# Kernel optimization log

Measured on AMD Instinct MI355X. Metric: run time of the kernel, lower is better.

Reference implementation:

```python
import jax, jax.numpy as jnp
import numpy as np

N_Q = 8
N_LAYERS = 3
SCALE = np.pi / 2


def _apply_1q(state, gate, q):
    # state: (B, 2,...,2) [N_Q qubit axes]; gate: (2,2) shared or (B,2,2) batched
    B = state.shape[0]
    s = jnp.moveaxis(state, 1 + q, 1).reshape(B, 2, -1)
    if gate.ndim == 2:
        s = jnp.einsum('ij,bjk->bik', gate, s)
    else:
        s = jnp.einsum('bij,bjk->bik', gate, s)
    s = s.reshape((B,) + (2,) * N_Q)
    return jnp.moveaxis(s, 1, 1 + q)


def _apply_cnot(state, c, t):
    # flip target axis within the control=1 slice
    s = jnp.moveaxis(state, (1 + c, 1 + t), (1, 2))
    s = jnp.concatenate([s[:, :1], jnp.flip(s[:, 1:], axis=2)], axis=1)
    return jnp.moveaxis(s, (1, 2), (1 + c, 1 + t))


def _ry(theta):
    # RY(t) = [[cos(t/2), -sin(t/2)], [sin(t/2), cos(t/2)]]; theta: (...,)
    c = jnp.cos(theta / 2)
    s = jnp.sin(theta / 2)
    m = jnp.stack([jnp.stack([c, -s], -1), jnp.stack([s, c], -1)], -2)
    return m.astype(jnp.complex64)


def _rz(phi):
    # RZ(p) = diag(exp(-ip/2), exp(ip/2))
    e = jnp.exp(-0.5j * phi.astype(jnp.complex64))
    z = jnp.zeros_like(e)
    return jnp.stack([jnp.stack([e, z], -1), jnp.stack([z, jnp.conj(e)], -1)], -2)


def _circuit(angles, theta, phi):
    # angles: (B, N_Q); theta, phi: (N_LAYERS, N_Q) -> Z expectations (B, N_Q)
    B = angles.shape[0]
    state = jnp.zeros((B, 2 ** N_Q), jnp.complex64).at[:, 0].set(1.0)
    state = state.reshape((B,) + (2,) * N_Q)
    enc = _ry(angles)  # (B, N_Q, 2, 2), batch-dependent encoding gates
    for q in range(N_Q):
        state = _apply_1q(state, enc[:, q], q)
    ryg = _ry(theta)  # (L, N_Q, 2, 2)
    rzg = _rz(phi)
    for l in range(N_LAYERS):
        for q in range(N_Q):
            state = _apply_1q(state, ryg[l, q], q)
        for q in range(N_Q):
            state = _apply_cnot(state, q, (q + 1) % N_Q)
        for q in range(N_Q):
            state = _apply_1q(state, rzg[l, q], q)
    probs = state.real ** 2 + state.imag ** 2  # (B, 2,...,2)
    z = []
    for q in range(N_Q):
        p = jnp.moveaxis(probs, 1 + q, 1).reshape(B, 2, -1).sum(-1)
        z.append(p[:, 0] - p[:, 1])
    return jnp.stack(z, axis=1)  # (B, N_Q)


def setup_inputs() -> dict:
    key = jax.random.key(0)
    ks = jax.random.split(key, 5)
    B, D, H = 16384, 256, 128
    x = jax.random.normal(ks[0], (B, D), dtype=jnp.float32)
    theta = jax.random.normal(ks[1], (N_LAYERS, N_Q), dtype=jnp.float32) * 0.1
    phi = jax.random.normal(ks[2], (N_LAYERS, N_Q), dtype=jnp.float32) * 0.1
    W1 = jax.random.normal(ks[3], (N_Q, H), dtype=jnp.float32) * (1.0 / np.sqrt(N_Q))
    b1 = jnp.zeros((H,), jnp.float32)
    W2 = jax.random.normal(ks[4], (H, D), dtype=jnp.float32) * (1.0 / np.sqrt(H))
    b2 = jnp.zeros((D,), jnp.float32)
    return {"x": x, "theta": theta, "phi": phi, "W1": W1, "b1": b1, "W2": W2, "b2": b2}


def reference(x, theta, phi, W1, b1, W2, b2):
    # per-sample min-max normalization (original calls _amplitude_encode on x[i:i+1])
    fmin = x.min(axis=1, keepdims=True)
    fmax = x.max(axis=1, keepdims=True)
    angles = (x[:, :N_Q] - fmin) / (fmax - fmin + 1e-8) * SCALE
    q = _circuit(angles, theta, phi)  # (B, 8) Pauli-Z expectations
    h = jax.nn.relu(q @ W1 + b1)
    transformed = h @ W2 + b2
    return x + transformed
```

## Files before the change

### kernel.cpp

```cpp
#include <hip/hip_runtime.h>
#include <hip/hip_bf16.h>

typedef __attribute__((ext_vector_type(8))) short short8;
typedef __attribute__((ext_vector_type(4))) float float4v;

#define PSTRIDE   260
#define PSISTRIDE 264
#define HSTRIDE   136

__device__ __forceinline__ float shflx(float v, int m) {
    return __shfl_xor(v, m, 64);
}

__device__ __forceinline__ unsigned short f2bf(float f) {
    union { __hip_bfloat16 h; unsigned short u; } cv;
    cv.h = __float2bfloat16(f);
    return cv.u;
}

__global__ __launch_bounds__(256) void vqc_build_u_kernel(
    const float* __restrict__ theta,
    const float* __restrict__ phi,
    const float* __restrict__ W2,
    unsigned short* __restrict__ Bmat,
    unsigned short* __restrict__ W2T)
{
    const int b = blockIdx.x;
    if (b >= 64) {
        const int k0 = (b - 64) * 4;
        const int n = threadIdx.x;
        ushort4 pk;
        pk.x = f2bf(W2[(k0 + 0) * 256 + n]);
        pk.y = f2bf(W2[(k0 + 1) * 256 + n]);
        pk.z = f2bf(W2[(k0 + 2) * 256 + n]);
        pk.w = f2bf(W2[(k0 + 3) * 256 + n]);
        *reinterpret_cast<ushort4*>(W2T + n * 128 + k0) = pk;
        return;
    }
    const int lane = threadIdx.x & 63;
    const int j = (b << 2) + (threadIdx.x >> 6);

    float re[4], im[4];
    #pragma unroll
    for (int jj = 0; jj < 4; ++jj) {
        re[jj] = (lane * 4 + jj == j) ? 1.f : 0.f;
        im[jj] = 0.f;
    }

    for (int l = 0; l < 3; ++l) {
        #pragma unroll
        for (int q = 0; q < 6; ++q) {
            float th = 0.5f * theta[l * 8 + q];
            float ct = __cosf(th), st = __sinf(th);
            float sg = ((lane >> (5 - q)) & 1) ? st : -st;
            const int m = 1 << (5 - q);
            #pragma unroll
            for (int jj = 0; jj < 4; ++jj) {
                float orr = shflx(re[jj], m), oi = shflx(im[jj], m);
                re[jj] = fmaf(ct, re[jj], sg * orr);
                im[jj] = fmaf(ct, im[jj], sg * oi);
            }
        }
        {
            float th = 0.5f * theta[l * 8 + 6];
            float ct = __cosf(th), st = __sinf(th);
            #pragma unroll
            for (int jj = 0; jj < 2; ++jj) {
                float r0 = re[jj], i0 = im[jj], r1 = re[jj + 2], i1 = im[jj + 2];
                re[jj]     = fmaf(ct, r0, -st * r1);
                im[jj]     = fmaf(ct, i0, -st * i1);
                re[jj + 2] = fmaf(ct, r1,  st * r0);
                im[jj + 2] = fmaf(ct, i1,  st * i0);
            }
        }
        {
            float th = 0.5f * theta[l * 8 + 7];
            float ct = __cosf(th), st = __sinf(th);
            #pragma unroll
            for (int jj = 0; jj < 4; jj += 2) {
                float r0 = re[jj], i0 = im[jj], r1 = re[jj + 1], i1 = im[jj + 1];
                re[jj]     = fmaf(ct, r0, -st * r1);
                im[jj]     = fmaf(ct, i0, -st * i1);
                re[jj + 1] = fmaf(ct, r1,  st * r0);
                im[jj + 1] = fmaf(ct, i1,  st * i0);
            }
        }
        #pragma unroll
        for (int q = 0; q < 5; ++q) {
            const int tm = 1 << (4 - q);
            const bool cb = (lane >> (5 - q)) & 1;
            #pragma unroll
            for (int jj = 0; jj < 4; ++jj) {
                float orr = shflx(re[jj], tm), oi = shflx(im[jj], tm);
                re[jj] = cb ? orr : re[jj];
                im[jj] = cb ? oi  : im[jj];
            }
        }
        {   const bool cb = lane & 1;
            float t;
            t = re[0]; re[0] = cb ? re[2] : re[0]; re[2] = cb ? t : re[2];
            t = im[0]; im[0] = cb ? im[2] : im[0]; im[2] = cb ? t : im[2];
            t = re[1]; re[1] = cb ? re[3] : re[1]; re[3] = cb ? t : re[3];
            t = im[1]; im[1] = cb ? im[3] : im[1]; im[3] = cb ? t : im[3];
        }
        {   float t;
            t = re[2]; re[2] = re[3]; re[3] = t;
            t = im[2]; im[2] = im[3]; im[3] = t;
        }
        {
            re[1] = shflx(re[1], 32); im[1] = shflx(im[1], 32);
            re[3] = shflx(re[3], 32); im[3] = shflx(im[3], 32);
        }
        float al = 0.f;
        #pragma unroll
        for (int q = 0; q < 6; ++q) {
            float h = 0.5f * phi[l * 8 + q];
            al += ((lane >> (5 - q)) & 1) ? h : -h;
        }
        float h6 = 0.5f * phi[l * 8 + 6], h7 = 0.5f * phi[l * 8 + 7];
        float ajs[4] = { al - h6 - h7, al - h6 + h7, al + h6 - h7, al + h6 + h7 };
        #pragma unroll
        for (int jj = 0; jj < 4; ++jj) {
            float cc = __cosf(ajs[jj]), sn = __sinf(ajs[jj]);
            float r = re[jj], i = im[jj];
            re[jj] = r * cc - i * sn;
            im[jj] = fmaf(r, sn, i * cc);
        }
    }

    #pragma unroll
    for (int jj = 0; jj < 4; ++jj) {
        int kp = lane * 4 + jj;
        Bmat[(size_t)kp * 256 + j]         = f2bf(re[jj]);
        Bmat[(size_t)(kp + 256) * 256 + j] = f2bf(im[jj]);
    }
}

__global__ __launch_bounds__(256) void vqc_mega_kernel(
    const float* __restrict__ x,
    const unsigned short* __restrict__ Bmat,
    const unsigned short* __restrict__ W2T,
    const float* __restrict__ W1,
    const float* __restrict__ b1,
    const float* __restrict__ b2,
    float* __restrict__ out,
    int B)
{
    __shared__ __align__(16) char smem[32 * PSTRIDE * 4];
    __shared__ float z_lds[32][8];
    float (*p_lds)[PSTRIDE] = (float(*)[PSTRIDE])smem;
    unsigned short (*psi_lds)[PSISTRIDE] = (unsigned short(*)[PSISTRIDE])smem;
    unsigned short (*h_lds)[HSTRIDE] = (unsigned short(*)[HSTRIDE])smem;

    const int t = threadIdx.x;
    const int lane = t & 63;
    const int w = t >> 6;
    const int c = lane & 15;
    const int quad = lane >> 4;
    const int s0 = blockIdx.x * 32;

    {
        const int g = t >> 3;
        const int sub = t & 7;
        const float4* xr = reinterpret_cast<const float4*>(x + (size_t)(s0 + g) * 256) + sub * 8;
        float4 v0 = xr[0], v1 = xr[1], v2 = xr[2], v3 = xr[3];
        float4 v4 = xr[4], v5 = xr[5], v6 = xr[6], v7 = xr[7];
        float mn = fminf(fminf(fminf(v0.x, v0.y), fminf(v0.z, v0.w)),
                         fminf(fminf(v1.x, v1.y), fminf(v1.z, v1.w)));
        mn = fminf(mn, fminf(fminf(fminf(v2.x, v2.y), fminf(v2.z, v2.w)),
                             fminf(fminf(v3.x, v3.y), fminf(v3.z, v3.w))));
        mn = fminf(mn, fminf(fminf(fminf(v4.x, v4.y), fminf(v4.z, v4.w)),
                             fminf(fminf(v5.x, v5.y), fminf(v5.z, v5.w))));
        mn = fminf(mn, fminf(fminf(fminf(v6.x, v6.y), fminf(v6.z, v6.w)),
                             fminf(fminf(v7.x, v7.y), fminf(v7.z, v7.w))));
        float mx = fmaxf(fmaxf(fmaxf(v0.x, v0.y), fmaxf(v0.z, v0.w)),
                         fmaxf(fmaxf(v1.x, v1.y), fmaxf(v1.z, v1.w)));
        mx = fmaxf(mx, fmaxf(fmaxf(fmaxf(v2.x, v2.y), fmaxf(v2.z, v2.w)),
                             fmaxf(fmaxf(v3.x, v3.y), fmaxf(v3.z, v3.w))));
        mx = fmaxf(mx, fmaxf(fmaxf(fmaxf(v4.x, v4.y), fmaxf(v4.z, v4.w)),
                             fmaxf(fmaxf(v5.x, v5.y), fmaxf(v5.z, v5.w))));
        mx = fmaxf(mx, fmaxf(fmaxf(fmaxf(v6.x, v6.y), fmaxf(v6.z, v6.w)),
                             fmaxf(fmaxf(v7.x, v7.y), fmaxf(v7.z, v7.w))));
        #pragma unroll
        for (int m = 1; m < 8; m <<= 1) {
            mn = fminf(mn, shflx(mn, m));
            mx = fmaxf(mx, shflx(mx, m));
        }
        const float scale = 0.78539816339744831f / (mx - mn + 1e-8f);

        const int base = lane & 56;
        float xq[8];
        xq[0] = __shfl(v0.x, base); xq[1] = __shfl(v0.y, base);
        xq[2] = __shfl(v0.z, base); xq[3] = __shfl(v0.w, base);
        xq[4] = __shfl(v1.x, base); xq[5] = __shfl(v1.y, base);
        xq[6] = __shfl(v1.z, base); xq[7] = __shfl(v1.w, base);

        float cq[8], sq[8];
        #pragma unroll
        for (int q = 0; q < 8; ++q) {
            float a = (xq[q] - mn) * scale;
            cq[q] = __cosf(a);
            sq[q] = __sinf(a);
        }
        float pref = ((sub >> 2) & 1 ? sq[0] : cq[0]) *
                     ((sub >> 1) & 1 ? sq[1] : cq[1]) *
                     ((sub >> 0) & 1 ? sq[2] : cq[2]);
        float p1[2], p2[4], p3[8], p4[16];
        p1[0] = pref * cq[3]; p1[1] = pref * sq[3];
        #pragma unroll
        for (int i = 0; i < 2; ++i) { p2[2*i] = p1[i] * cq[4]; p2[2*i+1] = p1[i] * sq[4]; }
        #pragma unroll
        for (int i = 0; i < 4; ++i) { p3[2*i] = p2[i] * cq[5]; p3[2*i+1] = p2[i] * sq[5]; }
        #pragma unroll
        for (int i = 0; i < 8; ++i) { p4[2*i] = p3[i] * cq[6]; p4[2*i+1] = p3[i] * sq[6]; }
        ushort2* dst = reinterpret_cast<ushort2*>(&psi_lds[g][sub * 32]);
        #pragma unroll
        for (int i = 0; i < 16; ++i) {
            ushort2 pk;
            pk.x = f2bf(p4[i] * cq[7]);
            pk.y = f2bf(p4[i] * sq[7]);
            dst[i] = pk;
        }
    }
    __syncthreads();

    float4v acc[2][8];
    #pragma unroll
    for (int h = 0; h < 2; ++h)
        #pragma unroll
        for (int tt = 0; tt < 8; ++tt)
            acc[h][tt] = (float4v){0.f, 0.f, 0.f, 0.f};

    #pragma unroll
    for (int kk = 0; kk < 8; ++kk) {
        const int ko = kk * 32 + quad * 8;
        short8 a0 = *(const short8*)(&psi_lds[c][ko]);
        short8 a1 = *(const short8*)(&psi_lds[16 + c][ko]);
        #pragma unroll
        for (int tt = 0; tt < 4; ++tt) {
            const int nr = (w * 4 + tt) * 16 + c;
            short8 bre = *(const short8*)(Bmat + (size_t)nr * 256 + ko);
            short8 bim = *(const short8*)(Bmat + (size_t)(nr + 256) * 256 + ko);
            acc[0][tt]     = __builtin_amdgcn_mfma_f32_16x16x32_bf16(a0, bre, acc[0][tt], 0, 0, 0);
            acc[1][tt]     = __builtin_amdgcn_mfma_f32_16x16x32_bf16(a1, bre, acc[1][tt], 0, 0, 0);
            acc[0][tt + 4] = __builtin_amdgcn_mfma_f32_16x16x32_bf16(a0, bim, acc[0][tt + 4], 0, 0, 0);
            acc[1][tt + 4] = __builtin_amdgcn_mfma_f32_16x16x32_bf16(a1, bim, acc[1][tt + 4], 0, 0, 0);
        }
    }
    __syncthreads();

    #pragma unroll
    for (int h = 0; h < 2; ++h)
        #pragma unroll
        for (int tt = 0; tt < 4; ++tt) {
            const int n = (w * 4 + tt) * 16 + c;
            #pragma unroll
            for (int r = 0; r < 4; ++r) {
                const int m = h * 16 + quad * 4 + r;
                const float pr = acc[h][tt][r], pi = acc[h][tt + 4][r];
                p_lds[m][n] = pr * pr + pi * pi;
            }
        }
    __syncthreads();

    {
        const int m = t >> 3, q = t & 7, sh = 7 - q;
        const float4* prow = (const float4*)&p_lds[m][0];
        float zv = 0.f;
        #pragma unroll 8
        for (int n4 = 0; n4 < 64; ++n4) {
            float4 pv = prow[n4];
            const int n = n4 * 4;
            zv += (((n + 0) >> sh) & 1) ? -pv.x : pv.x;
            zv += (((n + 1) >> sh) & 1) ? -pv.y : pv.y;
            zv += (((n + 2) >> sh) & 1) ? -pv.z : pv.z;
            zv += (((n + 3) >> sh) & 1) ? -pv.w : pv.w;
        }
        z_lds[m][q] = zv;
    }
    __syncthreads();

    {
        const int j = t & 127, ig = t >> 7;
        float w1v[8];
        #pragma unroll
        for (int q = 0; q < 8; ++q) w1v[q] = W1[q * 128 + j];
        const float b1v = b1[j];
        #pragma unroll
        for (int ii = 0; ii < 16; ++ii) {
            const int i = ig * 16 + ii;
            float a = b1v;
            #pragma unroll
            for (int q = 0; q < 8; ++q) a = fmaf(z_lds[i][q], w1v[q], a);
            h_lds[i][j] = f2bf(fmaxf(a, 0.f));
        }
    }
    __syncthreads();

    float4v acc2[2][4];
    #pragma unroll
    for (int h = 0; h < 2; ++h)
        #pragma unroll
        for (int tt = 0; tt < 4; ++tt)
            acc2[h][tt] = (float4v){0.f, 0.f, 0.f, 0.f};

    #pragma unroll
    for (int kk = 0; kk < 4; ++kk) {
        const int ko = kk * 32 + quad * 8;
        short8 a0 = *(const short8*)(&h_lds[c][ko]);
        short8 a1 = *(const short8*)(&h_lds[16 + c][ko]);
        #pragma unroll
        for (int tt = 0; tt < 4; ++tt) {
            const int nr = (w * 4 + tt) * 16 + c;
            short8 bw = *(const short8*)(W2T + (size_t)nr * 128 + ko);
            acc2[0][tt] = __builtin_amdgcn_mfma_f32_16x16x32_bf16(a0, bw, acc2[0][tt], 0, 0, 0);
            acc2[1][tt] = __builtin_amdgcn_mfma_f32_16x16x32_bf16(a1, bw, acc2[1][tt], 0, 0, 0);
        }
    }

    #pragma unroll
    for (int h = 0; h < 2; ++h)
        #pragma unroll
        for (int tt = 0; tt < 4; ++tt) {
            const int n = (w * 4 + tt) * 16 + c;
            const float b2v = b2[n];
            #pragma unroll
            for (int r = 0; r < 4; ++r) {
                const int m = h * 16 + quad * 4 + r;
                const size_t idx = (size_t)(s0 + m) * 256 + n;
                out[idx] = x[idx] + b2v + acc2[h][tt][r];
            }
        }
}

extern "C" void kernel_launch(void* const* d_in, const int* in_sizes, int n_in,
                              void* d_out, int out_size, void* d_ws, size_t ws_size,
                              hipStream_t stream) {
    const float* x     = (const float*)d_in[0];
    const float* theta = (const float*)d_in[1];
    const float* phi   = (const float*)d_in[2];
    const float* W1    = (const float*)d_in[3];
    const float* b1    = (const float*)d_in[4];
    const float* W2    = (const float*)d_in[5];
    const float* b2    = (const float*)d_in[6];
    float* out = (float*)d_out;
    const int B = in_sizes[0] / 256;

    unsigned short* Bmat = (unsigned short*)d_ws;
    unsigned short* W2T  = Bmat + 512 * 256;

    vqc_build_u_kernel<<<dim3(96), dim3(256), 0, stream>>>(theta, phi, W2, Bmat, W2T);
    vqc_mega_kernel<<<dim3(B / 32), dim3(256), 0, stream>>>(
        x, Bmat, W2T, W1, b1, b2, out, B);
}
```

Before: 108.2 us.

## Process 64 samples per 1024-thread block and restructure Z reduction

```diff
diff --git a/kernel.cpp b/kernel.cpp
--- a/kernel.cpp
+++ b/kernel.cpp
@@ -4,9 +4,10 @@
 typedef __attribute__((ext_vector_type(8))) short short8;
 typedef __attribute__((ext_vector_type(4))) float float4v;
 
-#define PSTRIDE   260
-#define PSISTRIDE 264
-#define HSTRIDE   136
+#define NS    64
+#define PSTR  264
+#define HSTR  136
+#define ZPSTR 68
 
 __device__ __forceinline__ float shflx(float v, int m) {
     return __shfl_xor(v, m, 64);
@@ -16,6 +17,12 @@
     union { __hip_bfloat16 h; unsigned short u; } cv;
     cv.h = __float2bfloat16(f);
     return cv.u;
+}
+
+__device__ __forceinline__ float bfbits(unsigned int u) {
+    union { unsigned int u; float f; } cv;
+    cv.u = u;
+    return cv.f;
 }
 
 __global__ __launch_bounds__(256) void vqc_build_u_kernel(
@@ -61,8 +68,7 @@
                 im[jj] = fmaf(ct, im[jj], sg * oi);
             }
         }
-        {
-            float th = 0.5f * theta[l * 8 + 6];
+        {   float th = 0.5f * theta[l * 8 + 6];
             float ct = __cosf(th), st = __sinf(th);
             #pragma unroll
             for (int jj = 0; jj < 2; ++jj) {
@@ -73,8 +79,7 @@
                 im[jj + 2] = fmaf(ct, i1,  st * i0);
             }
         }
-        {
-            float th = 0.5f * theta[l * 8 + 7];
+        {   float th = 0.5f * theta[l * 8 + 7];
             float ct = __cosf(th), st = __sinf(th);
             #pragma unroll
             for (int jj = 0; jj < 4; jj += 2) {
@@ -107,8 +112,7 @@
             t = re[2]; re[2] = re[3]; re[3] = t;
             t = im[2]; im[2] = im[3]; im[3] = t;
         }
-        {
-            re[1] = shflx(re[1], 32); im[1] = shflx(im[1], 32);
+        {   re[1] = shflx(re[1], 32); im[1] = shflx(im[1], 32);
             re[3] = shflx(re[3], 32); im[3] = shflx(im[3], 32);
         }
         float al = 0.f;
@@ -136,59 +140,50 @@
     }
 }
 
-__global__ __launch_bounds__(256) void vqc_mega_kernel(
+__global__ __launch_bounds__(1024) void vqc_mega_kernel(
     const float* __restrict__ x,
     const unsigned short* __restrict__ Bmat,
     const unsigned short* __restrict__ W2T,
     const float* __restrict__ W1,
     const float* __restrict__ b1,
     const float* __restrict__ b2,
-    float* __restrict__ out,
-    int B)
+    float* __restrict__ out)
 {
-    __shared__ __align__(16) char smem[32 * PSTRIDE * 4];
-    __shared__ float z_lds[32][8];
-    float (*p_lds)[PSTRIDE] = (float(*)[PSTRIDE])smem;
-    unsigned short (*psi_lds)[PSISTRIDE] = (unsigned short(*)[PSISTRIDE])smem;
-    unsigned short (*h_lds)[HSTRIDE] = (unsigned short(*)[HSTRIDE])smem;
+    __shared__ __align__(16) unsigned short region[NS * PSTR];
+    __shared__ __align__(16) float zp_lds[NS * ZPSTR];
+    __shared__ float z_lds[NS][8];
+
+    unsigned short (*psi)[PSTR]  = (unsigned short(*)[PSTR])region;
+    unsigned short (*hmat)[HSTR] = (unsigned short(*)[HSTR])region;
 
     const int t = threadIdx.x;
     const int lane = t & 63;
     const int w = t >> 6;
     const int c = lane & 15;
     const int quad = lane >> 4;
-    const int s0 = blockIdx.x * 32;
+    const int s0 = blockIdx.x * NS;
 
     {
-        const int g = t >> 3;
-        const int sub = t & 7;
-        const float4* xr = reinterpret_cast<const float4*>(x + (size_t)(s0 + g) * 256) + sub * 8;
+        const int g = t >> 4;
+        const int sub = t & 15;
+        const float4* xr = reinterpret_cast<const float4*>(x + (size_t)(s0 + g) * 256) + sub * 4;
         float4 v0 = xr[0], v1 = xr[1], v2 = xr[2], v3 = xr[3];
-        float4 v4 = xr[4], v5 = xr[5], v6 = xr[6], v7 = xr[7];
         float mn = fminf(fminf(fminf(v0.x, v0.y), fminf(v0.z, v0.w)),
                          fminf(fminf(v1.x, v1.y), fminf(v1.z, v1.w)));
         mn = fminf(mn, fminf(fminf(fminf(v2.x, v2.y), fminf(v2.z, v2.w)),
                              fminf(fminf(v3.x, v3.y), fminf(v3.z, v3.w))));
-        mn = fminf(mn, fminf(fminf(fminf(v4.x, v4.y), fminf(v4.z, v4.w)),
-                             fminf(fminf(v5.x, v5.y), fminf(v5.z, v5.w))));
-        mn = fminf(mn, fminf(fminf(fminf(v6.x, v6.y), fminf(v6.z, v6.w)),
-                             fminf(fminf(v7.x, v7.y), fminf(v7.z, v7.w))));
         float mx = fmaxf(fmaxf(fmaxf(v0.x, v0.y), fmaxf(v0.z, v0.w)),
                          fmaxf(fmaxf(v1.x, v1.y), fmaxf(v1.z, v1.w)));
         mx = fmaxf(mx, fmaxf(fmaxf(fmaxf(v2.x, v2.y), fmaxf(v2.z, v2.w)),
                              fmaxf(fmaxf(v3.x, v3.y), fmaxf(v3.z, v3.w))));
-        mx = fmaxf(mx, fmaxf(fmaxf(fmaxf(v4.x, v4.y), fmaxf(v4.z, v4.w)),
-                             fmaxf(fmaxf(v5.x, v5.y), fmaxf(v5.z, v5.w))));
-        mx = fmaxf(mx, fmaxf(fmaxf(fmaxf(v6.x, v6.y), fmaxf(v6.z, v6.w)),
-                             fmaxf(fmaxf(v7.x, v7.y), fmaxf(v7.z, v7.w))));
-        #pragma unroll
-        for (int m = 1; m < 8; m <<= 1) {
+        #pragma unroll
+        for (int m = 1; m < 16; m <<= 1) {
             mn = fminf(mn, shflx(mn, m));
             mx = fmaxf(mx, shflx(mx, m));
         }
         const float scale = 0.78539816339744831f / (mx - mn + 1e-8f);
 
-        const int base = lane & 56;
+        const int base = lane & 48;
         float xq[8];
         xq[0] = __shfl(v0.x, base); xq[1] = __shfl(v0.y, base);
         xq[2] = __shfl(v0.z, base); xq[3] = __shfl(v0.w, base);
@@ -202,80 +197,105 @@
             cq[q] = __cosf(a);
             sq[q] = __sinf(a);
         }
-        float pref = ((sub >> 2) & 1 ? sq[0] : cq[0]) *
-                     ((sub >> 1) & 1 ? sq[1] : cq[1]) *
-                     ((sub >> 0) & 1 ? sq[2] : cq[2]);
-        float p1[2], p2[4], p3[8], p4[16];
-        p1[0] = pref * cq[3]; p1[1] = pref * sq[3];
-        #pragma unroll
-        for (int i = 0; i < 2; ++i) { p2[2*i] = p1[i] * cq[4]; p2[2*i+1] = p1[i] * sq[4]; }
-        #pragma unroll
-        for (int i = 0; i < 4; ++i) { p3[2*i] = p2[i] * cq[5]; p3[2*i+1] = p2[i] * sq[5]; }
-        #pragma unroll
-        for (int i = 0; i < 8; ++i) { p4[2*i] = p3[i] * cq[6]; p4[2*i+1] = p3[i] * sq[6]; }
-        ushort2* dst = reinterpret_cast<ushort2*>(&psi_lds[g][sub * 32]);
-        #pragma unroll
-        for (int i = 0; i < 16; ++i) {
-            ushort2 pk;
-            pk.x = f2bf(p4[i] * cq[7]);
-            pk.y = f2bf(p4[i] * sq[7]);
-            dst[i] = pk;
-        }
-    }
-    __syncthreads();
-
-    float4v acc[2][8];
-    #pragma unroll
-    for (int h = 0; h < 2; ++h)
-        #pragma unroll
-        for (int tt = 0; tt < 8; ++tt)
-            acc[h][tt] = (float4v){0.f, 0.f, 0.f, 0.f};
-
+        float pref = ((sub & 8) ? sq[0] : cq[0]) *
+                     ((sub & 4) ? sq[1] : cq[1]) *
+                     ((sub & 2) ? sq[2] : cq[2]) *
+                     ((sub & 1) ? sq[3] : cq[3]);
+        float p1[2], p2[4], p3[8];
+        p1[0] = pref * cq[4]; p1[1] = pref * sq[4];
+        #pragma unroll
+        for (int i = 0; i < 2; ++i) { p2[2*i] = p1[i] * cq[5]; p2[2*i+1] = p1[i] * sq[5]; }
+        #pragma unroll
+        for (int i = 0; i < 4; ++i) { p3[2*i] = p2[i] * cq[6]; p3[2*i+1] = p2[i] * sq[6]; }
+        #pragma unroll
+        for (int i = 0; i < 4; ++i) {
+            ushort4 pk;
+            pk.x = f2bf(p3[2*i]     * cq[7]);
+            pk.y = f2bf(p3[2*i]     * sq[7]);
+            pk.z = f2bf(p3[2*i + 1] * cq[7]);
+            pk.w = f2bf(p3[2*i + 1] * sq[7]);
+            *reinterpret_cast<ushort4*>(&psi[g][sub * 16 + 4 * i]) = pk;
+        }
+    }
+    __syncthreads();
+
+    float4v accre[4], accim[4];
+    #pragma unroll
+    for (int mt = 0; mt < 4; ++mt) {
+        accre[mt] = (float4v){0.f, 0.f, 0.f, 0.f};
+        accim[mt] = (float4v){0.f, 0.f, 0.f, 0.f};
+    }
     #pragma unroll
     for (int kk = 0; kk < 8; ++kk) {
         const int ko = kk * 32 + quad * 8;
-        short8 a0 = *(const short8*)(&psi_lds[c][ko]);
-        short8 a1 = *(const short8*)(&psi_lds[16 + c][ko]);
-        #pragma unroll
-        for (int tt = 0; tt < 4; ++tt) {
-            const int nr = (w * 4 + tt) * 16 + c;
-            short8 bre = *(const short8*)(Bmat + (size_t)nr * 256 + ko);
-            short8 bim = *(const short8*)(Bmat + (size_t)(nr + 256) * 256 + ko);
-            acc[0][tt]     = __builtin_amdgcn_mfma_f32_16x16x32_bf16(a0, bre, acc[0][tt], 0, 0, 0);
-            acc[1][tt]     = __builtin_amdgcn_mfma_f32_16x16x32_bf16(a1, bre, acc[1][tt], 0, 0, 0);
-            acc[0][tt + 4] = __builtin_amdgcn_mfma_f32_16x16x32_bf16(a0, bim, acc[0][tt + 4], 0, 0, 0);
-            acc[1][tt + 4] = __builtin_amdgcn_mfma_f32_16x16x32_bf16(a1, bim, acc[1][tt + 4], 0, 0, 0);
-        }
-    }
-    __syncthreads();
-
-    #pragma unroll
-    for (int h = 0; h < 2; ++h)
-        #pragma unroll
-        for (int tt = 0; tt < 4; ++tt) {
-            const int n = (w * 4 + tt) * 16 + c;
-            #pragma unroll
-            for (int r = 0; r < 4; ++r) {
-                const int m = h * 16 + quad * 4 + r;
-                const float pr = acc[h][tt][r], pi = acc[h][tt + 4][r];
-                p_lds[m][n] = pr * pr + pi * pi;
-            }
-        }
-    __syncthreads();
-
-    {
-        const int m = t >> 3, q = t & 7, sh = 7 - q;
-        const float4* prow = (const float4*)&p_lds[m][0];
+        short8 a0 = *(const short8*)(&psi[c][ko]);
+        short8 a1 = *(const short8*)(&psi[16 + c][ko]);
+        short8 a2 = *(const short8*)(&psi[32 + c][ko]);
+        short8 a3 = *(const short8*)(&psi[48 + c][ko]);
+        short8 bre = *(const short8*)(Bmat + (size_t)(w * 16 + c) * 256 + ko);
+        short8 bim = *(const short8*)(Bmat + (size_t)(256 + w * 16 + c) * 256 + ko);
+        accre[0] = __builtin_amdgcn_mfma_f32_16x16x32_bf16(a0, bre, accre[0], 0, 0, 0);
+        accre[1] = __builtin_amdgcn_mfma_f32_16x16x32_bf16(a1, bre, accre[1], 0, 0, 0);
+        accre[2] = __builtin_amdgcn_mfma_f32_16x16x32_bf16(a2, bre, accre[2], 0, 0, 0);
+        accre[3] = __builtin_amdgcn_mfma_f32_16x16x32_bf16(a3, bre, accre[3], 0, 0, 0);
+        accim[0] = __builtin_amdgcn_mfma_f32_16x16x32_bf16(a0, bim, accim[0], 0, 0, 0);
+        accim[1] = __builtin_amdgcn_mfma_f32_16x16x32_bf16(a1, bim, accim[1], 0, 0, 0);
+        accim[2] = __builtin_amdgcn_mfma_f32_16x16x32_bf16(a2, bim, accim[2], 0, 0, 0);
+        accim[3] = __builtin_amdgcn_mfma_f32_16x16x32_bf16(a3, bim, accim[3], 0, 0, 0);
+    }
+    __syncthreads();
+
+    #pragma unroll
+    for (int mt = 0; mt < 4; ++mt)
+        #pragma unroll
+        for (int r = 0; r < 4; ++r) {
+            const int m = mt * 16 + quad * 4 + r;
+            const float pr = accre[mt][r], pi = accim[mt][r];
+            psi[m][w * 16 + c] = f2bf(pr * pr + pi * pi);
+        }
+    __syncthreads();
+
+    if (t < 512) {
+        const int m = t >> 3, h = t & 7;
+        const uint4* pu = (const uint4*)(&psi[m][h * 32]);
+        float s[8], d6s = 0.f, d7s = 0.f;
+        #pragma unroll
+        for (int i = 0; i < 4; ++i) {
+            uint4 u = pu[i];
+            {   float e0 = bfbits(u.x << 16), e1 = bfbits(u.x & 0xffff0000u);
+                float e2 = bfbits(u.y << 16), e3 = bfbits(u.y & 0xffff0000u);
+                float a01 = e0 + e1, a23 = e2 + e3;
+                s[2*i] = a01 + a23;
+                d6s += a01 - a23;
+                d7s += (e0 - e1) + (e2 - e3);
+            }
+            {   float e0 = bfbits(u.z << 16), e1 = bfbits(u.z & 0xffff0000u);
+                float e2 = bfbits(u.w << 16), e3 = bfbits(u.w & 0xffff0000u);
+                float a01 = e0 + e1, a23 = e2 + e3;
+                s[2*i+1] = a01 + a23;
+                d6s += a01 - a23;
+                d7s += (e0 - e1) + (e2 - e3);
+            }
+        }
+        float t01 = s[0] + s[1], t23 = s[2] + s[3], t45 = s[4] + s[5], t67 = s[6] + s[7];
+        float u03 = t01 + t23, u47 = t45 + t67;
+        float S  = u03 + u47;
+        float S3 = u03 - u47;
+        float S4 = (t01 - t23) + (t45 - t67);
+        float S5 = (s[0]-s[1]) + (s[2]-s[3]) + (s[4]-s[5]) + (s[6]-s[7]);
+        float* zr = &zp_lds[m * ZPSTR + h * 8];
+        zr[0] = (h & 4) ? -S : S;
+        zr[1] = (h & 2) ? -S : S;
+        zr[2] = (h & 1) ? -S : S;
+        zr[3] = S3; zr[4] = S4; zr[5] = S5; zr[6] = d6s; zr[7] = d7s;
+    }
+    __syncthreads();
+
+    if (t < 512) {
+        const int m = t >> 3, q = t & 7;
         float zv = 0.f;
-        #pragma unroll 8
-        for (int n4 = 0; n4 < 64; ++n4) {
-            float4 pv = prow[n4];
-            const int n = n4 * 4;
-            zv += (((n + 0) >> sh) & 1) ? -pv.x : pv.x;
-            zv += (((n + 1) >> sh) & 1) ? -pv.y : pv.y;
-            zv += (((n + 2) >> sh) & 1) ? -pv.z : pv.z;
-            zv += (((n + 3) >> sh) & 1) ? -pv.w : pv.w;
-        }
+        #pragma unroll
+        for (int h = 0; h < 8; ++h) zv += zp_lds[m * ZPSTR + h * 8 + q];
         z_lds[m][q] = zv;
     }
     __syncthreads();
@@ -287,50 +307,45 @@
         for (int q = 0; q < 8; ++q) w1v[q] = W1[q * 128 + j];
         const float b1v = b1[j];
         #pragma unroll
-        for (int ii = 0; ii < 16; ++ii) {
-            const int i = ig * 16 + ii;
+        for (int ii = 0; ii < 8; ++ii) {
+            const int i = ig * 8 + ii;
             float a = b1v;
             #pragma unroll
             for (int q = 0; q < 8; ++q) a = fmaf(z_lds[i][q], w1v[q], a);
-            h_lds[i][j] = f2bf(fmaxf(a, 0.f));
-        }
-    }
-    __syncthreads();
-
-    float4v acc2[2][4];
-    #pragma unroll
-    for (int h = 0; h < 2; ++h)
-        #pragma unroll
-        for (int tt = 0; tt < 4; ++tt)
-            acc2[h][tt] = (float4v){0.f, 0.f, 0.f, 0.f};
-
+            hmat[i][j] = f2bf(fmaxf(a, 0.f));
+        }
+    }
+    __syncthreads();
+
+    float4v acc2[4];
+    #pragma unroll
+    for (int mt = 0; mt < 4; ++mt) acc2[mt] = (float4v){0.f, 0.f, 0.f, 0.f};
     #pragma unroll
     for (int kk = 0; kk < 4; ++kk) {
         const int ko = kk * 32 + quad * 8;
-        short8 a0 = *(const short8*)(&h_lds[c][ko]);
-        short8 a1 = *(const short8*)(&h_lds[16 + c][ko]);
-        #pragma unroll
-        for (int tt = 0; tt < 4; ++tt) {
-            const int nr = (w * 4 + tt) * 16 + c;
-            short8 bw = *(const short8*)(W2T + (size_t)nr * 128 + ko);
-            acc2[0][tt] = __builtin_amdgcn_mfma_f32_16x16x32_bf16(a0, bw, acc2[0][tt], 0, 0, 0);
-            acc2[1][tt] = __builtin_amdgcn_mfma_f32_16x16x32_bf16(a1, bw, acc2[1][tt], 0, 0, 0);
-        }
-    }
-
-    #pragma unroll
-    for (int h = 0; h < 2; ++h)
-        #pragma unroll
-        for (int tt = 0; tt < 4; ++tt) {
-            const int n = (w * 4 + tt) * 16 + c;
-            const float b2v = b2[n];
+        short8 a0 = *(const short8*)(&hmat[c][ko]);
+        short8 a1 = *(const short8*)(&hmat[16 + c][ko]);
+        short8 a2 = *(const short8*)(&hmat[32 + c][ko]);
+        short8 a3 = *(const short8*)(&hmat[48 + c][ko]);
+        short8 bw = *(const short8*)(W2T + (size_t)(w * 16 + c) * 128 + ko);
+        acc2[0] = __builtin_amdgcn_mfma_f32_16x16x32_bf16(a0, bw, acc2[0], 0, 0, 0);
+        acc2[1] = __builtin_amdgcn_mfma_f32_16x16x32_bf16(a1, bw, acc2[1], 0, 0, 0);
+        acc2[2] = __builtin_amdgcn_mfma_f32_16x16x32_bf16(a2, bw, acc2[2], 0, 0, 0);
+        acc2[3] = __builtin_amdgcn_mfma_f32_16x16x32_bf16(a3, bw, acc2[3], 0, 0, 0);
+    }
+
+    {
+        const int n = w * 16 + c;
+        const float b2v = b2[n];
+        #pragma unroll
+        for (int mt = 0; mt < 4; ++mt)
             #pragma unroll
             for (int r = 0; r < 4; ++r) {
-                const int m = h * 16 + quad * 4 + r;
+                const int m = mt * 16 + quad * 4 + r;
                 const size_t idx = (size_t)(s0 + m) * 256 + n;
-                out[idx] = x[idx] + b2v + acc2[h][tt][r];
-            }
-        }
+                out[idx] = x[idx] + b2v + acc2[mt][r];
+            }
+    }
 }
 
 extern "C" void kernel_launch(void* const* d_in, const int* in_sizes, int n_in,
@@ -350,6 +365,6 @@
     unsigned short* W2T  = Bmat + 512 * 256;
 
     vqc_build_u_kernel<<<dim3(96), dim3(256), 0, stream>>>(theta, phi, W2, Bmat, W2T);
-    vqc_mega_kernel<<<dim3(B / 32), dim3(256), 0, stream>>>(
-        x, Bmat, W2T, W1, b1, b2, out, B);
-}
+    vqc_mega_kernel<<<dim3(B / NS), dim3(1024), 0, stream>>>(
+        x, Bmat, W2T, W1, b1, b2, out);
+}
```

New measurement: 98.70 us. 1.1x faster.
